# Kernel tuning notes

Measured on AMD Instinct MI355X. Metric: run time of the kernel, lower is better.

The kernel has to match this reference:

```python
import jax, jax.numpy as jnp
import numpy as np

WS = 7  # window size of the inner WindowAttention
EPS = 1e-5


def pc_roll(xb, shifts, axis):
    """Per-channel circular roll of [B,C,H,W] along `axis` (2 or 3).
    torch.roll semantics: out[i] = in[(i - shift) % n]."""
    n = xb.shape[axis]
    idx = (jnp.arange(n)[None, :] - shifts[:, None]) % n  # [C, n]
    if axis == 2:
        idxb = jnp.broadcast_to(idx[None, :, :, None], xb.shape)
    else:
        idxb = jnp.broadcast_to(idx[None, :, None, :], xb.shape)
    return jnp.take_along_axis(xb, idxb, axis=axis)


def layernorm(x, w, b):
    m = x.mean(-1, keepdims=True)
    v = x.var(-1, keepdims=True)
    return (x - m) * jax.lax.rsqrt(v + EPS) * w + b


def batchnorm2d(x, g, b):
    # training-mode BN: batch statistics over (B,H,W) per channel
    m = x.mean(axis=(0, 2, 3), keepdims=True)
    v = x.var(axis=(0, 2, 3), keepdims=True)
    return (x - m) * jax.lax.rsqrt(v + EPS) * g[None, :, None, None] + b[None, :, None, None]


def conv1x1(x, w, b):
    # x: [B,C,H,W], w: [Cout,Cin]
    return jnp.einsum('bchw,oc->bohw', x, w) + b[None, :, None, None]


def window_attention(q, k, v):
    # single-head Swin-style window attention, 7x7 windows, no rel-pos bias
    B, C, H, W = q.shape
    nh, nw = H // WS, W // WS

    def part(t):  # [B,C,H,W] -> [B*nh*nw, WS*WS, C]
        t = t.reshape(B, C, nh, WS, nw, WS)
        return t.transpose(0, 2, 4, 3, 5, 1).reshape(B * nh * nw, WS * WS, C)

    qw, kw, vw = part(q), part(k), part(v)
    scale = C ** -0.5
    attn = jax.nn.softmax(jnp.einsum('wnc,wmc->wnm', qw, kw) * scale, axis=-1)
    out = jnp.einsum('wnm,wmc->wnc', attn, vw)
    out = out.reshape(B, nh, nw, WS, WS, C).transpose(0, 5, 1, 3, 2, 4).reshape(B, C, H, W)
    return out


def setup_inputs() -> dict:
    B, H, W, C = 32, 56, 56, 128
    N = H * W
    key = jax.random.key(0)
    ks = jax.random.split(key, 16)
    f32 = jnp.float32

    def lin_w(k, din, dout):
        return 0.02 * jax.random.normal(k, (din, dout), dtype=f32)

    conv_std = float(np.sqrt(2.0 / C))
    inp = {
        'x': jax.random.normal(ks[0], (B, N, C), dtype=f32),
        'fc1_w': lin_w(ks[1], C, C), 'fc1_b': jnp.zeros((C,), f32),
        'fc2_w': lin_w(ks[2], C, C), 'fc2_b': jnp.zeros((C,), f32),
        'fc3_w': lin_w(ks[3], C, C), 'fc3_b': jnp.zeros((C,), f32),
        'fc4_w': lin_w(ks[4], C, C), 'fc4_b': jnp.zeros((C,), f32),
        'fc5_w': lin_w(ks[5], 2 * C, C), 'fc5_b': jnp.zeros((C,), f32),
        'fc6_w': lin_w(ks[6], 2 * C, C), 'fc6_b': jnp.zeros((C,), f32),
        'ln_w': jnp.ones((2 * C,), f32), 'ln_b': jnp.zeros((2 * C,), f32),
        'q_w': conv_std * jax.random.normal(ks[7], (C, C), dtype=f32), 'q_b': jnp.zeros((C,), f32),
        'k_w': conv_std * jax.random.normal(ks[8], (C, C), dtype=f32), 'k_b': jnp.zeros((C,), f32),
        'v_w': conv_std * jax.random.normal(ks[9], (C, C), dtype=f32), 'v_b': jnp.zeros((C,), f32),
        'bn1_g': jnp.ones((C,), f32), 'bn1_b': jnp.zeros((C,), f32),
        'bn2_g': jnp.ones((C,), f32), 'bn2_b': jnp.zeros((C,), f32),
        'H': H, 'W': W,
    }
    return inp


def reference(x, fc1_w, fc1_b, fc2_w, fc2_b, fc3_w, fc3_b, fc4_w, fc4_b,
              fc5_w, fc5_b, fc6_w, fc6_b, ln_w, ln_b,
              q_w, q_b, k_w, k_b, v_w, v_b, bn1_g, bn1_b, bn2_g, bn2_b, H, W):
    B, N, C = x.shape
    shifts = jnp.arange(C)
    gelu = lambda t: jax.nn.gelu(t, approximate=False)

    def to_bchw(t):
        return t.transpose(0, 2, 1).reshape(B, C, H, W)

    def to_bnc(t):
        return t.reshape(B, C, N).transpose(0, 2, 1)

    # branch 1: roll +c along H -> fc1 -> GELU -> roll +c along W -> fc2
    h = to_bnc(pc_roll(to_bchw(x), shifts, axis=2))
    h = gelu(h @ fc1_w + fc1_b)
    h = to_bnc(pc_roll(to_bchw(h), shifts, axis=3))
    x_1 = h @ fc2_w + fc2_b

    # branch 2: roll -c along W -> fc3 -> GELU -> roll +c along H -> fc4
    h = to_bnc(pc_roll(to_bchw(x), -shifts, axis=3))
    h = gelu(h @ fc3_w + fc3_b)
    h = to_bnc(pc_roll(to_bchw(h), shifts, axis=2))
    x_2 = h @ fc4_w + fc4_b

    x_1 = x_1 + x
    x_2 = x_2 + x
    x1 = jnp.concatenate([x_1, x_2], axis=2)          # [B,N,2C]
    x1 = layernorm(x1, ln_w, ln_b)
    x1 = x1 @ fc5_w + fc5_b
    x1 = x1 + x

    # local-attention branch (DWConv module actually runs WindowAtten + BN + ReLU)
    xb = to_bchw(x)
    att = window_attention(conv1x1(xb, q_w, q_b), conv1x1(xb, k_w, k_b), conv1x1(xb, v_w, v_b))
    x2 = jax.nn.relu(batchnorm2d(att, bn1_g, bn1_b))  # DWConv forward
    x2 = jax.nn.relu(x2)                              # act2 (idempotent, kept for fidelity)
    x2 = batchnorm2d(x2, bn2_g, bn2_b)                # norm2
    x2 = x2.reshape(B, C, N).transpose(0, 2, 1)       # [B,N,C]

    x3 = jnp.concatenate([x1, x2], axis=2)            # [B,N,2C]
    return x3 @ fc6_w + fc6_b
```

## Files before the change

kernel.cpp:

```cpp
#include <hip/hip_runtime.h>
#include <hip/hip_bf16.h>
#include <cstdint>
#include <cstddef>

typedef __bf16 bf16_t;
typedef __bf16 bf16x8 __attribute__((ext_vector_type(8)));
typedef float f32x4 __attribute__((ext_vector_type(4)));

#define B_SZ 32
#define H_SZ 56
#define W_SZ 56
#define N_TOK 3136
#define CH 128
#define M_TOT 100352

#define WOFF_FC1 0
#define WOFF_FC2 16384
#define WOFF_FC3 32768
#define WOFF_FC4 49152
#define WOFF_FC5 65536
#define WOFF_FC6 98304
#define WOFF_QW  131072
#define WOFF_KW  147456
#define WOFF_VW  163840
#define WTOT     180224

enum { A_FLAT = 0, A_WROLL, A_LN, A_BN };
enum { E_BIAS = 0, E_GELU, E_RES };

__device__ __forceinline__ float bf2f(bf16_t v) { return (float)v; }
__device__ __forceinline__ unsigned short bfbits(float v) {
    bf16_t b = (bf16_t)v; unsigned short u; __builtin_memcpy(&u, &b, 2); return u;
}

__global__ __launch_bounds__(256)
void wcvt_k(const float* __restrict__ f1, const float* __restrict__ f2,
            const float* __restrict__ f3, const float* __restrict__ f4,
            const float* __restrict__ f5, const float* __restrict__ f6,
            const float* __restrict__ qw, const float* __restrict__ kw,
            const float* __restrict__ vw, bf16_t* __restrict__ wb)
{
    const int blk = blockIdx.x;
    const int tid = threadIdx.x;
    if (blk < 32) {
        __shared__ bf16_t T[64][72];
        const float* src; bf16_t* dst; int K, t;
        if (blk < 4)       { src = f1; dst = wb + WOFF_FC1; K = 128; t = blk; }
        else if (blk < 8)  { src = f2; dst = wb + WOFF_FC2; K = 128; t = blk - 4; }
        else if (blk < 12) { src = f3; dst = wb + WOFF_FC3; K = 128; t = blk - 8; }
        else if (blk < 16) { src = f4; dst = wb + WOFF_FC4; K = 128; t = blk - 12; }
        else if (blk < 24) { src = f5; dst = wb + WOFF_FC5; K = 256; t = blk - 16; }
        else               { src = f6; dst = wb + WOFF_FC6; K = 256; t = blk - 24; }
        const int ti = t >> 1;
        const int tj = t & 1;
        for (int it = tid; it < 64 * 16; it += 256) {
            const int r = it >> 4, c4 = it & 15;
            float4 u = *(const float4*)(src + (size_t)(ti * 64 + r) * 128 + tj * 64 + c4 * 4);
            T[c4 * 4 + 0][r] = (bf16_t)u.x;
            T[c4 * 4 + 1][r] = (bf16_t)u.y;
            T[c4 * 4 + 2][r] = (bf16_t)u.z;
            T[c4 * 4 + 3][r] = (bf16_t)u.w;
        }
        __syncthreads();
        for (int it = tid; it < 64 * 8; it += 256) {
            const int n = it >> 3, ck = it & 7;
            *(uint4*)(dst + (size_t)(tj * 64 + n) * K + ti * 64 + ck * 8) =
                *(const uint4*)(&T[n][ck * 8]);
        }
    } else {
        const float* src; bf16_t* dst;
        int t = blk - 32;
        if (t < 4)      { src = qw; dst = wb + WOFF_QW; }
        else if (t < 8) { src = kw; dst = wb + WOFF_KW; t -= 4; }
        else            { src = vw; dst = wb + WOFF_VW; t -= 8; }
        const int base = t * 4096 + tid * 16;
        float4 u0 = *(const float4*)(src + base);
        float4 u1 = *(const float4*)(src + base + 4);
        float4 u2 = *(const float4*)(src + base + 8);
        float4 u3 = *(const float4*)(src + base + 12);
        bf16_t o[16] = {(bf16_t)u0.x, (bf16_t)u0.y, (bf16_t)u0.z, (bf16_t)u0.w,
                        (bf16_t)u1.x, (bf16_t)u1.y, (bf16_t)u1.z, (bf16_t)u1.w,
                        (bf16_t)u2.x, (bf16_t)u2.y, (bf16_t)u2.z, (bf16_t)u2.w,
                        (bf16_t)u3.x, (bf16_t)u3.y, (bf16_t)u3.z, (bf16_t)u3.w};
        *(uint4*)(dst + base) = *(const uint4*)o;
        *(uint4*)(dst + base + 8) = *(const uint4*)(o + 8);
    }
}

__global__ __launch_bounds__(256)
void transpose_k(const float* __restrict__ x, bf16_t* __restrict__ xT)
{
    __shared__ bf16_t T[128][70];
    const int tid = threadIdx.x;
    const int mbase = blockIdx.x * 64;
    const int bimg = mbase / N_TOK;
    const int n0 = mbase - bimg * N_TOK;
    for (int idx = tid; idx < 64 * 32; idx += 256) {
        const int tok = idx >> 5, cg = idx & 31;
        float4 u = *(const float4*)(x + (size_t)(mbase + tok) * CH + cg * 4);
        T[cg * 4 + 0][tok] = (bf16_t)u.x;
        T[cg * 4 + 1][tok] = (bf16_t)u.y;
        T[cg * 4 + 2][tok] = (bf16_t)u.z;
        T[cg * 4 + 3][tok] = (bf16_t)u.w;
    }
    __syncthreads();
    const uint* T32 = (const uint*)&T[0][0];
    for (int idx = tid; idx < 128 * 8; idx += 256) {
        const int c = idx >> 3, chunk = idx & 7;
        uint4 o;
        o.x = T32[c * 35 + chunk * 4 + 0];
        o.y = T32[c * 35 + chunk * 4 + 1];
        o.z = T32[c * 35 + chunk * 4 + 2];
        o.w = T32[c * 35 + chunk * 4 + 3];
        *(uint4*)(xT + ((size_t)(bimg * 128 + c)) * N_TOK + n0 + chunk * 8) = o;
    }
}

template<int AMODE, int KHALVES, int EPI, int WDIR, int OTRANS, int OF32>
__global__ __launch_bounds__(256)
void gemm_k(const bf16_t* __restrict__ A0, const bf16_t* __restrict__ A1,
            const bf16_t* __restrict__ Wt, const float* __restrict__ bias,
            const float* __restrict__ resid,
            const float* __restrict__ rowst,
            const float* __restrict__ lnw, const float* __restrict__ lnb,
            const float* __restrict__ bnp,
            void* __restrict__ outv)
{
    __shared__ __align__(16) char smem[17920];
    bf16_t* As = (bf16_t*)smem;
    const int tid = threadIdx.x;
    const int mbase = blockIdx.x * 64;
    const int bimg = mbase / N_TOK;
    const int n0 = mbase - bimg * N_TOK;
    const int lane = tid & 63;
    const int wv = tid >> 6;
    const int qd = lane >> 4;
    const int mr = lane & 15;
    const int KS = 128 * KHALVES;

    f32x4 acc[4][2];
#pragma unroll
    for (int i = 0; i < 4; ++i)
#pragma unroll
        for (int j = 0; j < 2; ++j) { f32x4 z = {0.f,0.f,0.f,0.f}; acc[i][j] = z; }

    for (int kh = 0; kh < KHALVES; ++kh) {
        if (kh) __syncthreads();
        if (AMODE == A_FLAT || AMODE == A_WROLL) {
            for (int idx = tid; idx < 128 * 8; idx += 256) {
                const int c = idx >> 3, chunk = idx & 7;
                const int cm = (c >= 112) ? c - 112 : (c >= 56 ? c - 56 : c);
                const bf16_t* crow = A0 + ((size_t)(bimg * 128 + c)) * N_TOK;
                if (AMODE == A_FLAT) {
                    int t = n0 + chunk * 8 + N_TOK - 56 * cm;
                    if (t >= N_TOK) t -= N_TOK;
                    uint4 u = *(const uint4*)(crow + t);
                    const bf16_t* up = (const bf16_t*)&u;
#pragma unroll
                    for (int j = 0; j < 8; ++j) As[(chunk * 8 + j) * 136 + c] = up[j];
                } else {
                    const int nl = n0 + chunk * 8;
                    const int h = nl / 56;
                    const int w0 = nl - h * 56;
                    int ws = (WDIR > 0) ? (w0 + cm) : (w0 + 56 - cm);
                    if (ws >= 56) ws -= 56;
                    const bf16_t* hrow = crow + h * 56;
                    if (ws <= 48) {
                        uint4 u = *(const uint4*)(hrow + ws);
                        const bf16_t* up = (const bf16_t*)&u;
#pragma unroll
                        for (int j = 0; j < 8; ++j) As[(chunk * 8 + j) * 136 + c] = up[j];
                    } else {
#pragma unroll
                        for (int j = 0; j < 8; ++j) {
                            int wj = ws + j; if (wj >= 56) wj -= 56;
                            As[(chunk * 8 + j) * 136 + c] = hrow[wj];
                        }
                    }
                }
            }
        } else if (AMODE == A_LN) {
            for (int idx = tid; idx < 64 * 16; idx += 256) {
                const int row = idx >> 4, ck = idx & 15;
                const int rowg = mbase + row;
                const bf16_t* src = kh ? A1 : A0;
                uint4 u = *(const uint4*)(src + (size_t)rowg * CH + ck * 8);
                const bf16_t* up = (const bf16_t*)&u;
                const float mean = rowst[2 * rowg];
                const float rstd = rowst[2 * rowg + 1];
                const int cabs = kh * 128 + ck * 8;
                bf16_t t[8];
#pragma unroll
                for (int j = 0; j < 8; ++j) {
                    float v = (bf2f(up[j]) - mean) * rstd;
                    v = v * lnw[cabs + j] + lnb[cabs + j];
                    t[j] = (bf16_t)v;
                }
                *(uint4*)(&As[row * 136 + ck * 8]) = *(const uint4*)t;
            }
        } else {
            for (int idx = tid; idx < 64 * 16; idx += 256) {
                const int row = idx >> 4, ck = idx & 15;
                const int rowg = mbase + row;
                if (kh == 0) {
                    uint4 u = *(const uint4*)(A0 + (size_t)rowg * CH + ck * 8);
                    *(uint4*)(&As[row * 136 + ck * 8]) = u;
                } else {
                    uint4 u = *(const uint4*)(A1 + (size_t)rowg * CH + ck * 8);
                    const bf16_t* up = (const bf16_t*)&u;
                    bf16_t t[8];
#pragma unroll
                    for (int j = 0; j < 8; ++j) {
                        const int c = ck * 8 + j;
                        float z = fmaxf(0.f, bf2f(up[j]) * bnp[c] + bnp[128 + c]);
                        t[j] = (bf16_t)(z * bnp[256 + c] + bnp[384 + c]);
                    }
                    *(uint4*)(&As[row * 136 + ck * 8]) = *(const uint4*)t;
                }
            }
        }
        __syncthreads();
        const bf16_t* wbase = Wt + (size_t)(wv * 32 + mr) * KS + kh * 128 + qd * 8;
#pragma unroll
        for (int kt = 0; kt < 4; ++kt) {
            bf16x8 af[4], bfr[2];
#pragma unroll
            for (int mt = 0; mt < 4; ++mt)
                af[mt] = *(const bf16x8*)(&As[(mt * 16 + mr) * 136 + kt * 32 + qd * 8]);
#pragma unroll
            for (int nt = 0; nt < 2; ++nt)
                bfr[nt] = *(const bf16x8*)(wbase + (size_t)(nt * 16) * KS + kt * 32);
#pragma unroll
            for (int mt = 0; mt < 4; ++mt)
#pragma unroll
                for (int nt = 0; nt < 2; ++nt)
                    acc[mt][nt] = __builtin_amdgcn_mfma_f32_16x16x32_bf16(
                        af[mt], bfr[nt], acc[mt][nt], 0, 0, 0);
        }
    }
    if (OTRANS) {
        __syncthreads();
        uint* T32 = (uint*)smem;
#pragma unroll
        for (int mt = 0; mt < 4; ++mt)
#pragma unroll
            for (int nt = 0; nt < 2; ++nt) {
                const int col = wv * 32 + nt * 16 + mr;
                const float bb = bias[col];
#pragma unroll
                for (int rp = 0; rp < 2; ++rp) {
                    float v0 = acc[mt][nt][2 * rp] + bb;
                    float v1 = acc[mt][nt][2 * rp + 1] + bb;
                    if (EPI == E_GELU) {
                        v0 = 0.5f * v0 * (1.f + erff(v0 * 0.70710678118654752f));
                        v1 = 0.5f * v1 * (1.f + erff(v1 * 0.70710678118654752f));
                    }
                    T32[col * 35 + mt * 8 + qd * 2 + rp] =
                        (uint)bfbits(v0) | ((uint)bfbits(v1) << 16);
                }
            }
        __syncthreads();
        const int c = tid >> 1, half = tid & 1;
        uint r[16];
#pragma unroll
        for (int j = 0; j < 16; ++j) r[j] = T32[c * 35 + half * 16 + j];
        bf16_t* op = (bf16_t*)outv + ((size_t)(bimg * 128 + c)) * N_TOK + n0 + half * 32;
        uint4 o0 = {r[0], r[1], r[2], r[3]};
        uint4 o1 = {r[4], r[5], r[6], r[7]};
        uint4 o2 = {r[8], r[9], r[10], r[11]};
        uint4 o3 = {r[12], r[13], r[14], r[15]};
        ((uint4*)op)[0] = o0; ((uint4*)op)[1] = o1;
        ((uint4*)op)[2] = o2; ((uint4*)op)[3] = o3;
    } else {
#pragma unroll
        for (int mt = 0; mt < 4; ++mt)
#pragma unroll
            for (int nt = 0; nt < 2; ++nt) {
                const int col = wv * 32 + nt * 16 + mr;
                const float bb = bias[col];
#pragma unroll
                for (int r = 0; r < 4; ++r) {
                    const int rowg = mbase + mt * 16 + qd * 4 + r;
                    float v = acc[mt][nt][r] + bb;
                    if (EPI == E_GELU) v = 0.5f * v * (1.f + erff(v * 0.70710678118654752f));
                    if (EPI == E_RES)  v += resid[(size_t)rowg * CH + col];
                    if (OF32) ((float*)outv)[(size_t)rowg * CH + col] = v;
                    else ((bf16_t*)outv)[(size_t)rowg * CH + col] = (bf16_t)v;
                }
            }
    }
}

__global__ __launch_bounds__(256)
void qkv_k(const float* __restrict__ x, const bf16_t* __restrict__ wb,
           const float* __restrict__ qb, const float* __restrict__ kb,
           const float* __restrict__ vb,
           bf16_t* __restrict__ qo, bf16_t* __restrict__ ko, bf16_t* __restrict__ vo)
{
    __shared__ __align__(16) bf16_t As[64 * 136];
    const int tid = threadIdx.x;
    const int mbase = blockIdx.x * 64;
    const int lane = tid & 63;
    const int wv = tid >> 6;
    const int qd = lane >> 4;
    const int mr = lane & 15;

    for (int idx = tid; idx < 64 * 16; idx += 256) {
        const int row = idx >> 4, ck = idx & 15;
        const float* p = x + (size_t)(mbase + row) * CH + ck * 8;
        float4 u0 = *(const float4*)p;
        float4 u1 = *(const float4*)(p + 4);
        bf16_t t[8] = {(bf16_t)u0.x, (bf16_t)u0.y, (bf16_t)u0.z, (bf16_t)u0.w,
                       (bf16_t)u1.x, (bf16_t)u1.y, (bf16_t)u1.z, (bf16_t)u1.w};
        *(uint4*)(&As[row * 136 + ck * 8]) = *(const uint4*)t;
    }
    __syncthreads();
    bf16x8 af[4][4];
#pragma unroll
    for (int kt = 0; kt < 4; ++kt)
#pragma unroll
        for (int mt = 0; mt < 4; ++mt)
            af[kt][mt] = *(const bf16x8*)(&As[(mt * 16 + mr) * 136 + kt * 32 + qd * 8]);

    const int woffs[3] = {WOFF_QW, WOFF_KW, WOFF_VW};
    const float* bs3[3] = {qb, kb, vb};
    bf16_t* os3[3] = {qo, ko, vo};
#pragma unroll
    for (int s = 0; s < 3; ++s) {
        const bf16_t* wbase = wb + woffs[s] + (size_t)(wv * 32 + mr) * 128 + qd * 8;
        f32x4 acc[4][2];
#pragma unroll
        for (int i = 0; i < 4; ++i)
#pragma unroll
            for (int j = 0; j < 2; ++j) { f32x4 z = {0.f,0.f,0.f,0.f}; acc[i][j] = z; }
#pragma unroll
        for (int kt = 0; kt < 4; ++kt) {
            bf16x8 bfr[2];
#pragma unroll
            for (int nt = 0; nt < 2; ++nt)
                bfr[nt] = *(const bf16x8*)(wbase + (nt * 16) * 128 + kt * 32);
#pragma unroll
            for (int mt = 0; mt < 4; ++mt)
#pragma unroll
                for (int nt = 0; nt < 2; ++nt)
                    acc[mt][nt] = __builtin_amdgcn_mfma_f32_16x16x32_bf16(
                        af[kt][mt], bfr[nt], acc[mt][nt], 0, 0, 0);
        }
        bf16_t* out = os3[s];
#pragma unroll
        for (int mt = 0; mt < 4; ++mt)
#pragma unroll
            for (int nt = 0; nt < 2; ++nt) {
                const int col = wv * 32 + nt * 16 + mr;
                const float bb = bs3[s][col];
#pragma unroll
                for (int r = 0; r < 4; ++r) {
                    const int rowg = mbase + mt * 16 + qd * 4 + r;
                    out[(size_t)rowg * CH + col] = (bf16_t)(acc[mt][nt][r] + bb);
                }
            }
    }
}

__global__ __launch_bounds__(256)
void rowstats_k(const bf16_t* __restrict__ x1p, const bf16_t* __restrict__ x2p,
                float* __restrict__ rs)
{
    const int row = blockIdx.x * 4 + (threadIdx.x >> 6);
    const int lane = threadIdx.x & 63;
    const bf16_t* p1 = x1p + (size_t)row * CH + lane * 2;
    const bf16_t* p2 = x2p + (size_t)row * CH + lane * 2;
    float a0 = bf2f(p1[0]), a1 = bf2f(p1[1]);
    float b0 = bf2f(p2[0]), b1 = bf2f(p2[1]);
    float s = a0 + a1 + b0 + b1;
    float sq = a0 * a0 + a1 * a1 + b0 * b0 + b1 * b1;
#pragma unroll
    for (int off = 32; off > 0; off >>= 1) {
        s += __shfl_down(s, off);
        sq += __shfl_down(sq, off);
    }
    if (lane == 0) {
        float mean = s * (1.f / 256.f);
        float var = sq * (1.f / 256.f) - mean * mean;
        rs[2 * row] = mean;
        rs[2 * row + 1] = rsqrtf(var + 1e-5f);
    }
}

__global__ __launch_bounds__(256, 4)
void attn_k(const bf16_t* __restrict__ qg, const bf16_t* __restrict__ kg,
            const bf16_t* __restrict__ vg, bf16_t* __restrict__ og,
            float* __restrict__ partial)
{
    __shared__ __align__(16) char smem[35840];
    bf16_t* Vr = (bf16_t*)smem;
    bf16_t* Ps = (bf16_t*)smem;
    bf16_t* Vt = (bf16_t*)(smem + 17408);
    bf16_t* Os = (bf16_t*)smem;
    float* bnacc = (float*)(smem + 34816);

    const int tid = threadIdx.x;
    const int blk = blockIdx.x;
    const int b = blk >> 6;
    const int wy = (blk >> 3) & 7;
    const int wx = blk & 7;
    const int lane = tid & 63;
    const int wv = tid >> 6;
    const int qd = lane >> 4;
    const int mr = lane & 15;

    bnacc[tid] = 0.f;

    const int vck = tid & 15;
    const int vi0 = tid >> 4;
    uint4 vld[4];
#pragma unroll
    for (int it = 0; it < 4; ++it) {
        const int i = vi0 + it * 16;
        uint4 uv = {0, 0, 0, 0};
        if (i < 49) {
            const int n = (wy * 7 + i / 7) * 56 + wx * 7 + (i % 7);
            uv = *(const uint4*)(vg + ((size_t)b * N_TOK + n) * CH + vck * 8);
        }
        vld[it] = uv;
    }

    const int qrow = wv * 16 + mr;
    const int qc = qrow < 49 ? qrow : 48;
    const bf16_t* qptr = qg + ((size_t)b * N_TOK +
                               (wy * 7 + qc / 7) * 56 + wx * 7 + (qc % 7)) * CH + qd * 8;
    bf16x8 aq[4];
#pragma unroll
    for (int kt = 0; kt < 4; ++kt)
        aq[kt] = *(const bf16x8*)(qptr + kt * 32);

    f32x4 sacc[4];
#pragma unroll
    for (int nt = 0; nt < 4; ++nt) {
        const int krow = nt * 16 + mr;
        const int kc = krow < 49 ? krow : 48;
        const bf16_t* kptr = kg + ((size_t)b * N_TOK +
                                   (wy * 7 + kc / 7) * 56 + wx * 7 + (kc % 7)) * CH + qd * 8;
        f32x4 a = {0.f, 0.f, 0.f, 0.f};
#pragma unroll
        for (int kt = 0; kt < 4; ++kt) {
            bf16x8 bk = *(const bf16x8*)(kptr + kt * 32);
            a = __builtin_amdgcn_mfma_f32_16x16x32_bf16(aq[kt], bk, a, 0, 0, 0);
        }
        sacc[nt] = a;
    }

#pragma unroll
    for (int it = 0; it < 4; ++it)
        *(uint4*)(&Vr[(vi0 + it * 16) * 136 + vck * 8]) = vld[it];
    __syncthreads();

    const int vc = tid & 127, vhalf = tid >> 7;
    uint4 vreg[4];
#pragma unroll
    for (int jc = 0; jc < 4; ++jc) {
        bf16_t t[8];
#pragma unroll
        for (int jj = 0; jj < 8; ++jj)
            t[jj] = Vr[(vhalf * 32 + jc * 8 + jj) * 136 + vc];
        vreg[jc] = *(const uint4*)t;
    }
    __syncthreads();

#pragma unroll
    for (int jc = 0; jc < 4; ++jc)
        *(uint4*)(&Vt[vc * 68 + (vhalf * 4 + jc) * 8]) = vreg[jc];

    {
        const float SCALE = 0.088388347648318447f;
#pragma unroll
        for (int nt = 0; nt < 4; ++nt) {
            const bool bad = (nt * 16 + mr) > 48;
#pragma unroll
            for (int r = 0; r < 4; ++r)
                sacc[nt][r] = bad ? -1e30f : sacc[nt][r] * SCALE;
        }
        float pv[4][4];
        float inv[4];
#pragma unroll
        for (int r = 0; r < 4; ++r) {
            float m = fmaxf(fmaxf(sacc[0][r], sacc[1][r]), fmaxf(sacc[2][r], sacc[3][r]));
            m = fmaxf(m, __shfl_xor(m, 1));
            m = fmaxf(m, __shfl_xor(m, 2));
            m = fmaxf(m, __shfl_xor(m, 4));
            m = fmaxf(m, __shfl_xor(m, 8));
#pragma unroll
            for (int nt = 0; nt < 4; ++nt) pv[nt][r] = __expf(sacc[nt][r] - m);
            float s = (pv[0][r] + pv[1][r]) + (pv[2][r] + pv[3][r]);
            s += __shfl_xor(s, 1);
            s += __shfl_xor(s, 2);
            s += __shfl_xor(s, 4);
            s += __shfl_xor(s, 8);
            inv[r] = 1.f / s;
        }
#pragma unroll
        for (int nt = 0; nt < 4; ++nt)
#pragma unroll
            for (int r = 0; r < 4; ++r)
                Ps[(wv * 16 + qd * 4 + r) * 72 + nt * 16 + mr] = (bf16_t)(pv[nt][r] * inv[r]);
    }
    __syncthreads();

    bf16x8 ap[2];
    ap[0] = *(const bf16x8*)(&Ps[(wv * 16 + mr) * 72 + qd * 8]);
    ap[1] = *(const bf16x8*)(&Ps[(wv * 16 + mr) * 72 + 32 + qd * 8]);
    f32x4 oacc[8];
#pragma unroll
    for (int nt = 0; nt < 8; ++nt) {
        f32x4 a = {0.f, 0.f, 0.f, 0.f};
#pragma unroll
        for (int kt = 0; kt < 2; ++kt) {
            bf16x8 bv = *(const bf16x8*)(&Vt[(nt * 16 + mr) * 68 + kt * 32 + qd * 8]);
            a = __builtin_amdgcn_mfma_f32_16x16x32_bf16(ap[kt], bv, a, 0, 0, 0);
        }
        oacc[nt] = a;
    }

#pragma unroll
    for (int nt = 0; nt < 8; ++nt) {
        const int c = nt * 16 + mr;
        float s = 0.f, sq = 0.f;
#pragma unroll
        for (int r = 0; r < 4; ++r) {
            const int q = wv * 16 + qd * 4 + r;
            if (q < 49) { const float v = oacc[nt][r]; s += v; sq += v * v; }
        }
        s += __shfl_xor(s, 16); sq += __shfl_xor(sq, 16);
        s += __shfl_xor(s, 32); sq += __shfl_xor(sq, 32);
        if (qd == 0) { atomicAdd(&bnacc[c], s); atomicAdd(&bnacc[128 + c], sq); }
    }
    __syncthreads();

#pragma unroll
    for (int nt = 0; nt < 8; ++nt) {
        const int c = nt * 16 + mr;
#pragma unroll
        for (int r = 0; r < 4; ++r) {
            const int q = wv * 16 + qd * 4 + r;
            Os[q * 140 + c] = (bf16_t)oacc[nt][r];
        }
    }
    __syncthreads();

    for (int idx = tid; idx < 49 * 16; idx += 256) {
        const int row = idx >> 4, u = idx & 15;
        const int n = (wy * 7 + row / 7) * 56 + wx * 7 + (row % 7);
        *(uint4*)(og + ((size_t)b * N_TOK + n) * CH + u * 8) =
            *(const uint4*)(&Os[row * 140 + u * 8]);
    }
    partial[(size_t)blk * 256 + tid] = bnacc[tid];
}

__global__ __launch_bounds__(256)
void bnreduce_k(const float* __restrict__ partial, float* __restrict__ accum)
{
    const int t = threadIdx.x;
    const int r0 = blockIdx.x * 16;
    float s = 0.f;
#pragma unroll
    for (int r = 0; r < 16; ++r) s += partial[(size_t)(r0 + r) * 256 + t];
    atomicAdd(&accum[t], s);
}

__global__ __launch_bounds__(256)
void bnstats2_k(const bf16_t* __restrict__ att, const float* __restrict__ g1,
                const float* __restrict__ b1, float* __restrict__ accum)
{
    __shared__ float ls[256], lq[256];
    const int c = threadIdx.x & 127;
    const int half = threadIdx.x >> 7;
    const float m = accum[c] * (1.f / (float)M_TOT);
    const float var = accum[128 + c] * (1.f / (float)M_TOT) - m * m;
    const float rstd = rsqrtf(var + 1e-5f);
    const float scl = g1[c] * rstd;
    const float sh = b1[c] - m * scl;
    const size_t rowbase = (size_t)blockIdx.x * 196;
    float s = 0.f, sq = 0.f;
    for (int r = half; r < 196; r += 2) {
        float z = fmaxf(0.f, bf2f(att[(rowbase + r) * CH + c]) * scl + sh);
        s += z; sq += z * z;
    }
    ls[threadIdx.x] = s; lq[threadIdx.x] = sq;
    __syncthreads();
    if (threadIdx.x < 128) {
        atomicAdd(&accum[256 + c], ls[threadIdx.x] + ls[threadIdx.x + 128]);
        atomicAdd(&accum[384 + c], lq[threadIdx.x] + lq[threadIdx.x + 128]);
    }
}

__global__ void bnparams_k(const float* __restrict__ accum,
                           const float* __restrict__ g1, const float* __restrict__ b1,
                           const float* __restrict__ g2, const float* __restrict__ b2,
                           float* __restrict__ bnp)
{
    const int c = threadIdx.x;
    const float inv = 1.f / (float)M_TOT;
    float m1 = accum[c] * inv;
    float v1 = accum[128 + c] * inv - m1 * m1;
    float rs1 = rsqrtf(v1 + 1e-5f);
    float s1 = g1[c] * rs1;
    float sh1 = b1[c] - m1 * s1;
    float m2 = accum[256 + c] * inv;
    float v2 = accum[384 + c] * inv - m2 * m2;
    float rs2 = rsqrtf(v2 + 1e-5f);
    float s2 = g2[c] * rs2;
    float sh2 = b2[c] - m2 * s2;
    bnp[c] = s1; bnp[128 + c] = sh1; bnp[256 + c] = s2; bnp[384 + c] = sh2;
}

__global__ void zero_k(float* __restrict__ p) { p[threadIdx.x] = 0.f; }

extern "C" void kernel_launch(void* const* d_in, const int* in_sizes, int n_in,
                              void* d_out, int out_size, void* d_ws, size_t ws_size,
                              hipStream_t stream)
{
    (void)in_sizes; (void)n_in; (void)out_size; (void)ws_size;
    const float* x     = (const float*)d_in[0];
    const float* fc1_w = (const float*)d_in[1];
    const float* fc1_b = (const float*)d_in[2];
    const float* fc2_w = (const float*)d_in[3];
    const float* fc2_b = (const float*)d_in[4];
    const float* fc3_w = (const float*)d_in[5];
    const float* fc3_b = (const float*)d_in[6];
    const float* fc4_w = (const float*)d_in[7];
    const float* fc4_b = (const float*)d_in[8];
    const float* fc5_w = (const float*)d_in[9];
    const float* fc5_b = (const float*)d_in[10];
    const float* fc6_w = (const float*)d_in[11];
    const float* fc6_b = (const float*)d_in[12];
    const float* ln_w  = (const float*)d_in[13];
    const float* ln_b  = (const float*)d_in[14];
    const float* q_w   = (const float*)d_in[15];
    const float* q_b   = (const float*)d_in[16];
    const float* k_w   = (const float*)d_in[17];
    const float* k_b   = (const float*)d_in[18];
    const float* v_w   = (const float*)d_in[19];
    const float* v_b   = (const float*)d_in[20];
    const float* bn1_g = (const float*)d_in[21];
    const float* bn1_b = (const float*)d_in[22];
    const float* bn2_g = (const float*)d_in[23];
    const float* bn2_b = (const float*)d_in[24];

    char* ws = (char*)d_ws;
    const size_t SZB = (size_t)M_TOT * CH * sizeof(bf16_t);
    bf16_t* bufA = (bf16_t*)(ws);
    bf16_t* bufB = (bf16_t*)(ws + SZB);
    bf16_t* bufC = (bf16_t*)(ws + 2 * SZB);
    bf16_t* bufD = (bf16_t*)(ws + 3 * SZB);
    float*  rs   = (float*)(ws + 4 * SZB);
    float*  accum = (float*)(ws + 4 * SZB + (size_t)M_TOT * 2 * sizeof(float));
    float*  bnp  = accum + 512;
    float*  partial = bnp + 512;
    bf16_t* wbuf = (bf16_t*)(partial + 2048 * 256);

    const dim3 blk(256);
    const int GG = M_TOT / 64;

    zero_k<<<1, 512, 0, stream>>>(accum);
    wcvt_k<<<44, blk, 0, stream>>>(fc1_w, fc2_w, fc3_w, fc4_w, fc5_w, fc6_w,
                                   q_w, k_w, v_w, wbuf);
    transpose_k<<<GG, blk, 0, stream>>>(x, bufA);
    gemm_k<A_FLAT, 1, E_GELU, 0, 1, 0><<<GG, blk, 0, stream>>>(
        bufA, nullptr, wbuf + WOFF_FC1, fc1_b, nullptr, nullptr, nullptr, nullptr, nullptr, bufB);
    gemm_k<A_WROLL, 1, E_RES, -1, 0, 0><<<GG, blk, 0, stream>>>(
        bufB, nullptr, wbuf + WOFF_FC2, fc2_b, x, nullptr, nullptr, nullptr, nullptr, bufC);
    gemm_k<A_WROLL, 1, E_GELU, 1, 1, 0><<<GG, blk, 0, stream>>>(
        bufA, nullptr, wbuf + WOFF_FC3, fc3_b, nullptr, nullptr, nullptr, nullptr, nullptr, bufB);
    gemm_k<A_FLAT, 1, E_RES, 0, 0, 0><<<GG, blk, 0, stream>>>(
        bufB, nullptr, wbuf + WOFF_FC4, fc4_b, x, nullptr, nullptr, nullptr, nullptr, bufD);
    rowstats_k<<<M_TOT / 4, blk, 0, stream>>>(bufC, bufD, rs);
    gemm_k<A_LN, 2, E_RES, 0, 0, 0><<<GG, blk, 0, stream>>>(
        bufC, bufD, wbuf + WOFF_FC5, fc5_b, x, rs, ln_w, ln_b, nullptr, bufB);
    qkv_k<<<GG, blk, 0, stream>>>(x, wbuf, q_b, k_b, v_b, bufA, bufC, bufD);
    attn_k<<<B_SZ * 64, blk, 0, stream>>>(bufA, bufC, bufD, bufA, partial);
    bnreduce_k<<<128, blk, 0, stream>>>(partial, accum);
    bnstats2_k<<<512, blk, 0, stream>>>(bufA, bn1_g, bn1_b, accum);
    bnparams_k<<<1, 128, 0, stream>>>(accum, bn1_g, bn1_b, bn2_g, bn2_b, bnp);
    gemm_k<A_BN, 2, E_BIAS, 0, 0, 1><<<GG, blk, 0, stream>>>(
        bufB, bufA, wbuf + WOFF_FC6, fc6_b, nullptr, nullptr, nullptr, nullptr, bnp, d_out);
}
```

Measured before the change: 463.2 us.

## Swizzle GEMM A-tile LDS layout and transpose V directly in attention kernel

Applies an XOR swizzle to the 16-byte column groups of the A tile in shared memory for the GEMM and QKV kernels, which is meant to cut bank conflicts on both the transposed scalar stores and the MFMA fragment loads. In the attention kernel, V is written straight from registers into its transposed LDS layout, dropping the staging buffer and one barrier. This shrinks shared memory so launch bounds can be raised to 6 blocks per SM. The scalar transposed stores may still conflict, and the higher occupancy target may constrain registers.

```diff
diff --git a/kernel.cpp b/kernel.cpp
--- a/kernel.cpp
+++ b/kernel.cpp
@@ -32,6 +32,7 @@
 __device__ __forceinline__ unsigned short bfbits(float v) {
     bf16_t b = (bf16_t)v; unsigned short u; __builtin_memcpy(&u, &b, 2); return u;
 }
+__device__ __forceinline__ int aswz(int row, int g) { return g ^ ((row >> 3) & 7); }
 
 __global__ __launch_bounds__(256)
 void wcvt_k(const float* __restrict__ f1, const float* __restrict__ f2,
@@ -151,13 +152,17 @@
                 const int c = idx >> 3, chunk = idx & 7;
                 const int cm = (c >= 112) ? c - 112 : (c >= 56 ? c - 56 : c);
                 const bf16_t* crow = A0 + ((size_t)(bimg * 128 + c)) * N_TOK;
+                const int cg = c >> 3, co = c & 7;
                 if (AMODE == A_FLAT) {
                     int t = n0 + chunk * 8 + N_TOK - 56 * cm;
                     if (t >= N_TOK) t -= N_TOK;
                     uint4 u = *(const uint4*)(crow + t);
                     const bf16_t* up = (const bf16_t*)&u;
 #pragma unroll
-                    for (int j = 0; j < 8; ++j) As[(chunk * 8 + j) * 136 + c] = up[j];
+                    for (int j = 0; j < 8; ++j) {
+                        const int row = chunk * 8 + j;
+                        As[row * 136 + aswz(row, cg) * 8 + co] = up[j];
+                    }
                 } else {
                     const int nl = n0 + chunk * 8;
                     const int h = nl / 56;
@@ -169,12 +174,16 @@
                         uint4 u = *(const uint4*)(hrow + ws);
                         const bf16_t* up = (const bf16_t*)&u;
 #pragma unroll
-                        for (int j = 0; j < 8; ++j) As[(chunk * 8 + j) * 136 + c] = up[j];
+                        for (int j = 0; j < 8; ++j) {
+                            const int row = chunk * 8 + j;
+                            As[row * 136 + aswz(row, cg) * 8 + co] = up[j];
+                        }
                     } else {
 #pragma unroll
                         for (int j = 0; j < 8; ++j) {
                             int wj = ws + j; if (wj >= 56) wj -= 56;
-                            As[(chunk * 8 + j) * 136 + c] = hrow[wj];
+                            const int row = chunk * 8 + j;
+                            As[row * 136 + aswz(row, cg) * 8 + co] = hrow[wj];
                         }
                     }
                 }
@@ -196,7 +205,7 @@
                     v = v * lnw[cabs + j] + lnb[cabs + j];
                     t[j] = (bf16_t)v;
                 }
-                *(uint4*)(&As[row * 136 + ck * 8]) = *(const uint4*)t;
+                *(uint4*)(&As[row * 136 + aswz(row, ck) * 8]) = *(const uint4*)t;
             }
         } else {
             for (int idx = tid; idx < 64 * 16; idx += 256) {
@@ -204,7 +213,7 @@
                 const int rowg = mbase + row;
                 if (kh == 0) {
                     uint4 u = *(const uint4*)(A0 + (size_t)rowg * CH + ck * 8);
-                    *(uint4*)(&As[row * 136 + ck * 8]) = u;
+                    *(uint4*)(&As[row * 136 + aswz(row, ck) * 8]) = u;
                 } else {
                     uint4 u = *(const uint4*)(A1 + (size_t)rowg * CH + ck * 8);
                     const bf16_t* up = (const bf16_t*)&u;
@@ -215,7 +224,7 @@
                         float z = fmaxf(0.f, bf2f(up[j]) * bnp[c] + bnp[128 + c]);
                         t[j] = (bf16_t)(z * bnp[256 + c] + bnp[384 + c]);
                     }
-                    *(uint4*)(&As[row * 136 + ck * 8]) = *(const uint4*)t;
+                    *(uint4*)(&As[row * 136 + aswz(row, ck) * 8]) = *(const uint4*)t;
                 }
             }
         }
@@ -225,8 +234,10 @@
         for (int kt = 0; kt < 4; ++kt) {
             bf16x8 af[4], bfr[2];
 #pragma unroll
-            for (int mt = 0; mt < 4; ++mt)
-                af[mt] = *(const bf16x8*)(&As[(mt * 16 + mr) * 136 + kt * 32 + qd * 8]);
+            for (int mt = 0; mt < 4; ++mt) {
+                const int row = mt * 16 + mr;
+                af[mt] = *(const bf16x8*)(&As[row * 136 + aswz(row, kt * 4 + qd) * 8]);
+            }
 #pragma unroll
             for (int nt = 0; nt < 2; ++nt)
                 bfr[nt] = *(const bf16x8*)(wbase + (size_t)(nt * 16) * KS + kt * 32);
@@ -312,15 +323,17 @@
         float4 u1 = *(const float4*)(p + 4);
         bf16_t t[8] = {(bf16_t)u0.x, (bf16_t)u0.y, (bf16_t)u0.z, (bf16_t)u0.w,
                        (bf16_t)u1.x, (bf16_t)u1.y, (bf16_t)u1.z, (bf16_t)u1.w};
-        *(uint4*)(&As[row * 136 + ck * 8]) = *(const uint4*)t;
+        *(uint4*)(&As[row * 136 + aswz(row, ck) * 8]) = *(const uint4*)t;
     }
     __syncthreads();
     bf16x8 af[4][4];
 #pragma unroll
     for (int kt = 0; kt < 4; ++kt)
 #pragma unroll
-        for (int mt = 0; mt < 4; ++mt)
-            af[kt][mt] = *(const bf16x8*)(&As[(mt * 16 + mr) * 136 + kt * 32 + qd * 8]);
+        for (int mt = 0; mt < 4; ++mt) {
+            const int row = mt * 16 + mr;
+            af[kt][mt] = *(const bf16x8*)(&As[row * 136 + aswz(row, kt * 4 + qd) * 8]);
+        }
 
     const int woffs[3] = {WOFF_QW, WOFF_KW, WOFF_VW};
     const float* bs3[3] = {qb, kb, vb};
@@ -387,17 +400,16 @@
     }
 }
 
-__global__ __launch_bounds__(256, 4)
+__global__ __launch_bounds__(256, 6)
 void attn_k(const bf16_t* __restrict__ qg, const bf16_t* __restrict__ kg,
             const bf16_t* __restrict__ vg, bf16_t* __restrict__ og,
             float* __restrict__ partial)
 {
-    __shared__ __align__(16) char smem[35840];
-    bf16_t* Vr = (bf16_t*)smem;
-    bf16_t* Ps = (bf16_t*)smem;
-    bf16_t* Vt = (bf16_t*)(smem + 17408);
+    __shared__ __align__(16) char smem[27136];
+    bf16_t* Vt = (bf16_t*)smem;
+    bf16_t* Ps = (bf16_t*)(smem + 17408);
+    float* bnacc = (float*)(smem + 26112);
     bf16_t* Os = (bf16_t*)smem;
-    float* bnacc = (float*)(smem + 34816);
 
     const int tid = threadIdx.x;
     const int blk = blockIdx.x;
@@ -411,8 +423,8 @@
 
     bnacc[tid] = 0.f;
 
-    const int vck = tid & 15;
-    const int vi0 = tid >> 4;
+    const int vi0 = tid & 15;
+    const int vck = tid >> 4;
     uint4 vld[4];
 #pragma unroll
     for (int it = 0; it < 4; ++it) {
@@ -451,25 +463,13 @@
     }
 
 #pragma unroll
-    for (int it = 0; it < 4; ++it)
-        *(uint4*)(&Vr[(vi0 + it * 16) * 136 + vck * 8]) = vld[it];
-    __syncthreads();
-
-    const int vc = tid & 127, vhalf = tid >> 7;
-    uint4 vreg[4];
-#pragma unroll
-    for (int jc = 0; jc < 4; ++jc) {
-        bf16_t t[8];
-#pragma unroll
-        for (int jj = 0; jj < 8; ++jj)
-            t[jj] = Vr[(vhalf * 32 + jc * 8 + jj) * 136 + vc];
-        vreg[jc] = *(const uint4*)t;
-    }
-    __syncthreads();
-
-#pragma unroll
-    for (int jc = 0; jc < 4; ++jc)
-        *(uint4*)(&Vt[vc * 68 + (vhalf * 4 + jc) * 8]) = vreg[jc];
+    for (int it = 0; it < 4; ++it) {
+        const int i = vi0 + it * 16;
+        const bf16_t* vp = (const bf16_t*)&vld[it];
+#pragma unroll
+        for (int j = 0; j < 8; ++j)
+            Vt[(vck * 8 + j) * 68 + i] = vp[j];
+    }
 
     {
         const float SCALE = 0.088388347648318447f;
@@ -502,13 +502,13 @@
         for (int nt = 0; nt < 4; ++nt)
 #pragma unroll
             for (int r = 0; r < 4; ++r)
-                Ps[(wv * 16 + qd * 4 + r) * 72 + nt * 16 + mr] = (bf16_t)(pv[nt][r] * inv[r]);
+                Ps[(wv * 16 + qd * 4 + r) * 68 + nt * 16 + mr] = (bf16_t)(pv[nt][r] * inv[r]);
     }
     __syncthreads();
 
     bf16x8 ap[2];
-    ap[0] = *(const bf16x8*)(&Ps[(wv * 16 + mr) * 72 + qd * 8]);
-    ap[1] = *(const bf16x8*)(&Ps[(wv * 16 + mr) * 72 + 32 + qd * 8]);
+    ap[0] = *(const bf16x8*)(&Ps[(wv * 16 + mr) * 68 + qd * 8]);
+    ap[1] = *(const bf16x8*)(&Ps[(wv * 16 + mr) * 68 + 32 + qd * 8]);
     f32x4 oacc[8];
 #pragma unroll
     for (int nt = 0; nt < 8; ++nt) {
@@ -542,7 +542,7 @@
 #pragma unroll
         for (int r = 0; r < 4; ++r) {
             const int q = wv * 16 + qd * 4 + r;
-            Os[q * 140 + c] = (bf16_t)oacc[nt][r];
+            Os[q * 136 + c] = (bf16_t)oacc[nt][r];
         }
     }
     __syncthreads();
@@ -551,7 +551,7 @@
         const int row = idx >> 4, u = idx & 15;
         const int n = (wy * 7 + row / 7) * 56 + wx * 7 + (row % 7);
         *(uint4*)(og + ((size_t)b * N_TOK + n) * CH + u * 8) =
-            *(const uint4*)(&Os[row * 140 + u * 8]);
+            *(const uint4*)(&Os[row * 136 + u * 8]);
     }
     partial[(size_t)blk * 256 + tid] = bnacc[tid];
 }
```

Measured after the change: 464.1 us. Within noise of the previous version (+0.2%).
